# Performance work log

Measured on AMD Instinct MI355X. Metric: run time of the kernel, lower is better.

## Reference

```python
import jax, jax.numpy as jnp
import numpy as np

B, D, H, W = 32, 96, 96, 96
MAX_POINTS = 512
NUM_CLASSES = 512
# e3nn spherical-harmonic 'integral' normalization constants
C0 = 0.28209479177387814   # 1/(2*sqrt(pi))
C1 = 0.4886025119029199    # sqrt(3/(4*pi))
C2 = 0.6307831305050401    # sqrt(5/(4*pi))
SQ3 = 1.7320508075688772

# (multiplicity, irrep dim) blocks for each irreps layout
BLOCKS_IN = [(16, 1), (8, 3), (4, 5)]   # 16x0e + 8x1o + 4x2e = 60
BLOCKS_H1 = [(32, 1), (8, 3), (4, 5)]   # 76
BLOCKS_H2 = [(64, 1), (4, 3), (2, 5)]   # 86


def setup_inputs() -> dict:
    key = jax.random.key(0)
    ks = jax.random.split(key, 12)
    n = jax.random.normal
    return {
        "x": jax.random.uniform(ks[0], (B, 1, D, H, W), dtype=jnp.float32),
        "W1_0e": n(ks[1], (16, 32)), "W1_1o": n(ks[2], (8, 8)), "W1_2e": n(ks[3], (4, 4)),
        "W2_0e": n(ks[4], (32, 64)), "W2_1o": n(ks[5], (8, 4)), "W2_2e": n(ks[6], (4, 2)),
        "W3_0e": n(ks[7], (64, 128)),
        "fc1_w": n(ks[8], (128, 64)) * 0.05, "fc1_b": jnp.zeros((64,), jnp.float32),
        "fc2_w": n(ks[9], (64, NUM_CLASSES)) * 0.05, "fc2_b": jnp.zeros((NUM_CLASSES,), jnp.float32),
    }


def _topk_pointcloud(x):
    # topk sampling path: highest-density voxels (threshold filter is a no-op
    # for top-k when enough voxels pass, which holds here). x: (B,1,D,H,W)
    vol = x[:, 0]
    flat = vol.reshape(vol.shape[0], -1)
    vals, idx = jax.lax.top_k(flat, MAX_POINTS)          # (B,N)
    z = idx // (H * W)
    rem = idx % (H * W)
    y = rem // W
    xw = rem % W
    coords = jnp.stack([z, y, xw], axis=-1).astype(jnp.float32)  # (B,N,3)
    center = jnp.array([D, H, W], jnp.float32) / 2.0
    scale = float(max(D, H, W)) / 2.0
    points = (coords - center) / scale
    return points, vals


def _point_features(pts, vals):
    # pts: (B,N,3) normalized coords, vals: (B,N) densities -> (B,N,60)
    v = vals[..., None]
    denom = vals.sum(axis=1, keepdims=True)
    com = (pts * v).sum(axis=1) / jnp.maximum(denom, 1e-12)      # (B,3)
    c = pts - com[:, None, :]
    r = jnp.maximum(jnp.linalg.norm(c, axis=-1), 1e-6)           # r_safe (B,N)
    rr = r[..., None]
    d = c / rr                                                   # unit directions
    dx, dy, dz = d[..., 0], d[..., 1], d[..., 2]
    sh1 = C1 * d                                                 # l=1 SH, e3nn order (x,y,z)
    sh2 = C2 * jnp.stack([
        SQ3 * dx * dz,
        SQ3 * dx * dy,
        dy * dy - 0.5 * (dx * dx + dz * dz),
        SQ3 * dy * dz,
        0.5 * SQ3 * (dz * dz - dx * dx),
    ], axis=-1)                                                  # (B,N,5)
    l1pr = jnp.log1p(r)
    sh0 = jnp.full_like(vals, C0)
    scalars = jnp.stack([
        vals, r, sh0, vals * r, vals ** 2, l1pr, jnp.sqrt(vals + 1e-6),
        r ** 2, vals * sh0, jnp.exp(-r), vals ** 3, jnp.sqrt(r),
        vals * l1pr, jax.nn.sigmoid(vals), jax.nn.sigmoid(r), vals * r ** 2,
    ], axis=-1)                                                  # (B,N,16)
    vectors = jnp.concatenate([
        c, c * v, sh1, c * rr, d, d * v, c * v ** 2, sh1 * rr,
    ], axis=-1)                                                  # (B,N,24)
    tensors = jnp.concatenate([
        sh2, sh2 * v, sh2 * rr, sh2 * l1pr[..., None],
    ], axis=-1)                                                  # (B,N,20)
    return jnp.concatenate([scalars, vectors, tensors], axis=-1)


def _irreps_linear(feat, blocks, weights):
    # e3nn o3.Linear: block-diagonal per-irrep linear, one path per block,
    # path normalization 1/sqrt(mul_in). Blocks laid out mul-major.
    outs = []
    start = 0
    for (mul_in, dim), Wb in zip(blocks, weights):
        blk = feat[..., start:start + mul_in * dim]
        blk = blk.reshape(*feat.shape[:-1], mul_in, dim)
        out = jnp.einsum('bnui,uv->bnvi', blk, Wb) / np.sqrt(mul_in).astype(np.float32)
        outs.append(out.reshape(*feat.shape[:-1], -1))
        start += mul_in * dim
    return jnp.concatenate(outs, axis=-1)


def reference(x, W1_0e, W1_1o, W1_2e, W2_0e, W2_1o, W2_2e, W3_0e,
              fc1_w, fc1_b, fc2_w, fc2_b):
    pts, vals = _topk_pointcloud(x)
    feat = _point_features(pts, vals)                    # (B,512,60)
    h = _irreps_linear(feat, BLOCKS_IN, [W1_0e, W1_1o, W1_2e])   # (B,512,76)
    h = _irreps_linear(h, BLOCKS_H1, [W2_0e, W2_1o, W2_2e])      # (B,512,86)
    # layer3 -> 128x0e: only the 0e path exists, 1o/2e inputs are dropped
    h = _irreps_linear(h[..., :64], [(64, 1)], [W3_0e])          # (B,512,128)
    pooled = h.max(axis=1)                               # (B,128)
    hid = jax.nn.relu(pooled @ fc1_w + fc1_b)            # dropout is eval-mode identity
    logits = hid @ fc2_w + fc2_b
    return logits, feat
```

## Files before the change

kernel.cpp:

```cpp
#include <hip/hip_runtime.h>
#include <hip/hip_bf16.h>
#include <stdint.h>

#define NVOX   884736
#define NB     32
#define NPTS   512
#define CAP    4096
#define THRV   0.9990234375f
#define THR_TOP 0x3F7FFFFFu
#define BPB    216
#define SLOT   64
#define LBUF   80
#define NBUCK  128

#define C0c  0.28209479177387814f
#define C1c  0.4886025119029199f
#define C2c  0.6307831305050401f
#define SQ3c 1.7320508075688772f

typedef unsigned long long u64;
typedef unsigned int u32;

__global__ __launch_bounds__(256) void k_collect(const float* __restrict__ x,
                                                 u64* __restrict__ cand,
                                                 u32* __restrict__ counts) {
  const int b   = blockIdx.y;
  const int blk = blockIdx.x;
  const int tid = threadIdx.x;
  __shared__ u64 lbuf[LBUF];
  __shared__ int lcnt;
  if (tid == 0) lcnt = 0;
  __syncthreads();

  const float4* xb = reinterpret_cast<const float4*>(x + (size_t)b * NVOX);
  const int t0 = blk * 1024 + tid;
  float4 q[4];
  #pragma unroll
  for (int it = 0; it < 4; ++it) q[it] = xb[t0 + it * 256];

  #pragma unroll
  for (int it = 0; it < 4; ++it) {
    const float4 qq = q[it];
    const u32 base = (u32)(t0 + it * 256) * 4u;
    if (qq.x >= THRV) { int p = atomicAdd(&lcnt, 1); if (p < LBUF) lbuf[p] = ((u64)__float_as_uint(qq.x) << 32) | (u64)(~(base      )); }
    if (qq.y >= THRV) { int p = atomicAdd(&lcnt, 1); if (p < LBUF) lbuf[p] = ((u64)__float_as_uint(qq.y) << 32) | (u64)(~(base + 1u)); }
    if (qq.z >= THRV) { int p = atomicAdd(&lcnt, 1); if (p < LBUF) lbuf[p] = ((u64)__float_as_uint(qq.z) << 32) | (u64)(~(base + 2u)); }
    if (qq.w >= THRV) { int p = atomicAdd(&lcnt, 1); if (p < LBUF) lbuf[p] = ((u64)__float_as_uint(qq.w) << 32) | (u64)(~(base + 3u)); }
  }
  __syncthreads();

  const int slot = b * BPB + blk;
  const int n = lcnt;
  const int wn = (n <= SLOT) ? n : SLOT;
  if (tid < wn) cand[(size_t)slot * SLOT + tid] = lbuf[tid];
  if (tid == 0) counts[slot] = (n <= SLOT) ? (u32)n : (u32)(SLOT + 1);
}

__global__ __launch_bounds__(512) void k_select(const float* __restrict__ x,
                                                const u64* __restrict__ cand,
                                                const u32* __restrict__ counts,
                                                u64* __restrict__ sel,
                                                float* __restrict__ comvg) {
  const int b   = blockIdx.x;
  const int tid = threadIdx.x;

  __shared__ u64 lk[CAP];
  __shared__ u64 lk2[CAP];
  __shared__ u64 sk[NPTS];
  __shared__ u32 sA[256], sB[256];
  __shared__ u32 scnt[BPB], spref[BPB];
  __shared__ u32 bc[NBUCK], bbx[NBUCK], bp[NBUCK], bA[NBUCK], bB[NBUCK];
  __shared__ float rbuf[8][4];
  __shared__ int sbad, sC;
  __shared__ u32 sthr;

  u32 myc = 0;
  if (tid == 0) sbad = 0;
  if (tid < 256) { myc = (tid < BPB) ? counts[b * BPB + tid] : 0u; sA[tid] = myc; }
  __syncthreads();
  if (tid < BPB && myc > SLOT) atomicOr(&sbad, 1);
  u32 *ssrc = sA, *sdst = sB;
  for (int off = 1; off < 256; off <<= 1) {
    if (tid < 256) sdst[tid] = ssrc[tid] + ((tid >= off) ? ssrc[tid - off] : 0u);
    __syncthreads();
    u32* t = ssrc; ssrc = sdst; sdst = t;
  }
  const int total = (int)ssrc[255];
  if (tid < BPB) { scnt[tid] = myc; spref[tid] = ssrc[tid] - myc; }
  __syncthreads();

  int C;
  if (!sbad && total >= NPTS && total <= CAP) {
    C = total;
    for (int s = tid >> 1; s < BPB; s += 256) {
      const u32 c = scnt[s], p = spref[s];
      const u64* src = cand + (size_t)(b * BPB + s) * SLOT;
      for (u32 k = (u32)(tid & 1); k < c; k += 2) lk[p + k] = src[k];
    }
    __syncthreads();
  } else {
    u32* hist = reinterpret_cast<u32*>(lk);
    for (int i = tid; i < 4096; i += 512) hist[i] = 0u;
    __syncthreads();
    const u32* xb = reinterpret_cast<const u32*>(x) + (size_t)b * NVOX;
    for (int i = tid; i < NVOX; i += 512) {
      const u32 bits = xb[i];
      u32 key;
      if (bits >= 0x3F800000u) key = 0u;
      else { const u32 dd = THR_TOP - bits; key = dd >> 8; if (key > 4095u) key = 4095u; }
      atomicAdd(&hist[key], 1u);
    }
    __syncthreads();
    if (tid == 0) {
      u32 cum = 0; int kt = 4095;
      for (int k = 0; k < 4096; ++k) { cum += hist[k]; if (cum >= (u32)NPTS) { kt = k; break; } }
      sthr = (kt >= 4095) ? 0u : (0x3F800000u - ((u32)(kt + 1) << 8));
      sC = 0;
    }
    __syncthreads();
    const u32 thr = sthr;
    for (int i = tid; i < NVOX; i += 512) {
      const u32 bits = xb[i];
      if (bits >= thr) {
        const int p = atomicAdd(&sC, 1);
        if (p < CAP) lk[p] = ((u64)bits << 32) | (u64)(~(u32)i);
      }
    }
    __syncthreads();
    C = sC < CAP ? sC : CAP;
    __syncthreads();
  }

  if (tid < NBUCK) bc[tid] = 0u;
  __syncthreads();
  for (int i = tid; i < C; i += 512) {
    const u32 bits = (u32)(lk[i] >> 32);
    u32 bk = (THR_TOP - bits) >> 7; if (bk > (NBUCK - 1)) bk = NBUCK - 1;
    atomicAdd(&bc[bk], 1u);
  }
  __syncthreads();
  if (tid < NBUCK) bA[tid] = bc[tid];
  __syncthreads();
  u32 *bsrc = bA, *bdst = bB;
  for (int off = 1; off < NBUCK; off <<= 1) {
    if (tid < NBUCK) bdst[tid] = bsrc[tid] + ((tid >= off) ? bsrc[tid - off] : 0u);
    __syncthreads();
    u32* t = bsrc; bsrc = bdst; bdst = t;
  }
  if (tid < NBUCK) { bbx[tid] = bsrc[tid] - bc[tid]; bp[tid] = bsrc[tid] - bc[tid]; }
  __syncthreads();
  for (int i = tid; i < C; i += 512) {
    const u64 ki = lk[i];
    const u32 bits = (u32)(ki >> 32);
    u32 bk = (THR_TOP - bits) >> 7; if (bk > (NBUCK - 1)) bk = NBUCK - 1;
    const u32 p = atomicAdd(&bp[bk], 1u);
    lk2[p] = ki;
  }
  __syncthreads();
  for (int i = tid; i < C; i += 512) {
    const u64 ki = lk2[i];
    const u32 bits = (u32)(ki >> 32);
    u32 bk = (THR_TOP - bits) >> 7; if (bk > (NBUCK - 1)) bk = NBUCK - 1;
    const u32 lo = bbx[bk], hi = lo + bc[bk];
    int rank = (int)lo;
    for (u32 j = lo; j < hi; ++j) rank += (lk2[j] > ki) ? 1 : 0;
    if (rank < NPTS) sk[rank] = ki;
  }
  __syncthreads();

  const u64 key = sk[tid];
  sel[(size_t)b * NPTS + tid] = key;

  const u32 bits = (u32)(key >> 32);
  const u32 idx  = ~((u32)key);
  const float v  = __uint_as_float(bits);
  const u32 z = idx / 9216u, rem = idx % 9216u, yy = rem / 96u, xw = rem % 96u;
  const float p0 = ((float)z  - 48.f) / 48.f;
  const float p1 = ((float)yy - 48.f) / 48.f;
  const float p2 = ((float)xw - 48.f) / 48.f;
  float sv = v, s0 = p0 * v, s1 = p1 * v, s2 = p2 * v;
  for (int off = 32; off > 0; off >>= 1) {
    sv += __shfl_down(sv, off);
    s0 += __shfl_down(s0, off);
    s1 += __shfl_down(s1, off);
    s2 += __shfl_down(s2, off);
  }
  const int w = tid >> 6, ln = tid & 63;
  if (ln == 0) { rbuf[w][0] = sv; rbuf[w][1] = s0; rbuf[w][2] = s1; rbuf[w][3] = s2; }
  __syncthreads();
  if (tid == 0) {
    float tv = 0.f, t0s = 0.f, t1s = 0.f, t2s = 0.f;
    for (int wv = 0; wv < 8; ++wv) { tv += rbuf[wv][0]; t0s += rbuf[wv][1]; t1s += rbuf[wv][2]; t2s += rbuf[wv][3]; }
    const float dnm = fmaxf(tv, 1e-12f);
    comvg[b * 4 + 0] = t0s / dnm; comvg[b * 4 + 1] = t1s / dnm;
    comvg[b * 4 + 2] = t2s / dnm; comvg[b * 4 + 3] = 0.f;
  }
}

__global__ __launch_bounds__(512) void k_featpool(const u64* __restrict__ sel,
                                                  const float* __restrict__ comvg,
                                                  const float* __restrict__ W1,
                                                  const float* __restrict__ W2,
                                                  const float* __restrict__ W3,
                                                  float* __restrict__ ppart,
                                                  float* __restrict__ dout) {
  const int p8  = blockIdx.x;
  const int b   = blockIdx.y;
  const int tid = threadIdx.x;
  __shared__ float Tm[16 * 64];
  __shared__ float Ms[16 * 128];
  __shared__ __align__(16) float fs[64][20];
  __shared__ float pr[4][128];

  const float s1c = 1.0f / (4.0f * sqrtf(32.0f));
  for (int e = tid; e < 16 * 64; e += 512) {
    const int u = e >> 6, j = e & 63;
    float s = 0.f;
    for (int k = 0; k < 32; ++k) s += W1[u * 32 + k] * W2[k * 64 + j];
    Tm[e] = s * s1c;
  }
  __syncthreads();
  for (int e = tid; e < 16 * 128; e += 512) {
    const int u = e >> 7, vv = e & 127;
    float s = 0.f;
    for (int j = 0; j < 64; ++j) s += Tm[u * 64 + j] * W3[j * 128 + vv];
    Ms[e] = s * 0.125f;
  }

  const int pl = tid >> 3, cg = tid & 7;
  const int gp = b * NPTS + p8 * 64 + pl;
  const u64 key = sel[gp];
  const u32 bits = (u32)(key >> 32);
  const u32 idx  = ~((u32)key);
  const float v  = __uint_as_float(bits);
  const u32 z = idx / 9216u, rem = idx % 9216u, yy = rem / 96u, xw = rem % 96u;
  const float4 cm = reinterpret_cast<const float4*>(comvg)[b];
  const float c0 = ((float)z  - 48.f) / 48.f - cm.x;
  const float c1 = ((float)yy - 48.f) / 48.f - cm.y;
  const float c2 = ((float)xw - 48.f) / 48.f - cm.z;
  const float r = fmaxf(sqrtf(c0 * c0 + c1 * c1 + c2 * c2), 1e-6f);
  const float inv = 1.0f / r;
  const float d0 = c0 * inv, d1 = c1 * inv, d2 = c2 * inv;
  const float v2 = v * v;
  const float rr2 = r * r;
  const float l1 = log1pf(r);
  const float er = expf(-r);
  const float sgv = 1.0f / (1.0f + expf(-v));
  const float sgr = 1.0f / (1.0f + expf(-r));

  float f[60];
  f[0]=v;      f[1]=r;      f[2]=C0c;     f[3]=v*r;
  f[4]=v2;     f[5]=l1;     f[6]=sqrtf(v + 1e-6f); f[7]=rr2;
  f[8]=v*C0c;  f[9]=er;     f[10]=v2*v;   f[11]=sqrtf(r);
  f[12]=v*l1;  f[13]=sgv;   f[14]=sgr;    f[15]=v*rr2;
  f[16]=c0;        f[17]=c1;        f[18]=c2;
  f[19]=c0*v;      f[20]=c1*v;      f[21]=c2*v;
  f[22]=C1c*d0;    f[23]=C1c*d1;    f[24]=C1c*d2;
  f[25]=c0*r;      f[26]=c1*r;      f[27]=c2*r;
  f[28]=d0;        f[29]=d1;        f[30]=d2;
  f[31]=d0*v;      f[32]=d1*v;      f[33]=d2*v;
  f[34]=c0*v2;     f[35]=c1*v2;     f[36]=c2*v2;
  f[37]=C1c*d0*r;  f[38]=C1c*d1*r;  f[39]=C1c*d2*r;
  const float t0 = C2c * (SQ3c * d0 * d2);
  const float t1 = C2c * (SQ3c * d0 * d1);
  const float t2_ = C2c * (d1 * d1 - 0.5f * (d0 * d0 + d2 * d2));
  const float t3 = C2c * (SQ3c * d1 * d2);
  const float t4 = C2c * (0.5f * SQ3c * (d2 * d2 - d0 * d0));
  f[40]=t0;     f[41]=t1;     f[42]=t2_;     f[43]=t3;     f[44]=t4;
  f[45]=t0*v;   f[46]=t1*v;   f[47]=t2_*v;   f[48]=t3*v;   f[49]=t4*v;
  f[50]=t0*r;   f[51]=t1*r;   f[52]=t2_*r;   f[53]=t3*r;   f[54]=t4*r;
  f[55]=t0*l1;  f[56]=t1*l1;  f[57]=t2_*l1;  f[58]=t3*l1;  f[59]=t4*l1;

  float4* ob = reinterpret_cast<float4*>(dout + 16384 + (size_t)gp * 60);
  #pragma unroll
  for (int k = 0; k < 15; ++k)
    if ((k & 7) == cg) ob[k] = make_float4(f[4*k], f[4*k+1], f[4*k+2], f[4*k+3]);

  #pragma unroll
  for (int k = 0; k < 4; ++k)
    if (k == cg) *reinterpret_cast<float4*>(&fs[pl][k * 4]) =
        make_float4(f[4*k], f[4*k+1], f[4*k+2], f[4*k+3]);
  __syncthreads();

  const int g = tid >> 7, vv = tid & 127;
  float mreg[16];
  #pragma unroll
  for (int u = 0; u < 16; ++u) mreg[u] = Ms[u * 128 + vv];
  float pm = -3.4e38f;
  for (int n = g; n < 64; n += 4) {
    const float4 a0 = *reinterpret_cast<const float4*>(&fs[n][0]);
    const float4 a1 = *reinterpret_cast<const float4*>(&fs[n][4]);
    const float4 a2 = *reinterpret_cast<const float4*>(&fs[n][8]);
    const float4 a3 = *reinterpret_cast<const float4*>(&fs[n][12]);
    float acc = a0.x*mreg[0] + a0.y*mreg[1] + a0.z*mreg[2] + a0.w*mreg[3]
              + a1.x*mreg[4] + a1.y*mreg[5] + a1.z*mreg[6] + a1.w*mreg[7]
              + a2.x*mreg[8] + a2.y*mreg[9] + a2.z*mreg[10]+ a2.w*mreg[11]
              + a3.x*mreg[12]+ a3.y*mreg[13]+ a3.z*mreg[14]+ a3.w*mreg[15];
    pm = fmaxf(pm, acc);
  }
  pr[g][vv] = pm;
  __syncthreads();
  if (g == 0)
    ppart[((size_t)b * 8 + p8) * 128 + vv] =
        fmaxf(fmaxf(pr[0][vv], pr[1][vv]), fmaxf(pr[2][vv], pr[3][vv]));
}

__global__ __launch_bounds__(512) void k_head(const float* __restrict__ ppart,
                                              const float* __restrict__ fc1w,
                                              const float* __restrict__ fc1b,
                                              const float* __restrict__ fc2w,
                                              const float* __restrict__ fc2b,
                                              float* __restrict__ dout) {
  const int b = blockIdx.x;
  const int t = threadIdx.x;
  __shared__ float pl[128];
  __shared__ float hid[64];
  if (t < 128) {
    float m = -3.4e38f;
    #pragma unroll
    for (int k = 0; k < 8; ++k) m = fmaxf(m, ppart[((size_t)b * 8 + k) * 128 + t]);
    pl[t] = m;
  }
  __syncthreads();
  if (t < 64) {
    float sh = fc1b[t];
    for (int u = 0; u < 128; ++u) sh += pl[u] * fc1w[u * 64 + t];
    hid[t] = fmaxf(sh, 0.f);
  }
  __syncthreads();
  float sl = fc2b[t];
  for (int j = 0; j < 64; ++j) sl += hid[j] * fc2w[j * 512 + t];
  dout[b * 512 + t] = sl;
}

extern "C" void kernel_launch(void* const* d_in, const int* in_sizes, int n_in,
                              void* d_out, int out_size, void* d_ws, size_t ws_size,
                              hipStream_t stream) {
  const float* x    = (const float*)d_in[0];
  const float* W1   = (const float*)d_in[1];
  const float* W2   = (const float*)d_in[4];
  const float* W3   = (const float*)d_in[7];
  const float* fc1w = (const float*)d_in[8];
  const float* fc1b = (const float*)d_in[9];
  const float* fc2w = (const float*)d_in[10];
  const float* fc2b = (const float*)d_in[11];
  float* out = (float*)d_out;

  uint8_t* ws = (uint8_t*)d_ws;
  u32*   counts = (u32*)ws;
  u64*   cand   = (u64*)(ws + 0x10000);
  u64*   sel    = (u64*)(ws + 0x400000);
  float* comv   = (float*)(ws + 0x420000);
  float* ppart  = (float*)(ws + 0x421000);

  dim3 g1(BPB, NB);
  k_collect<<<g1, 256, 0, stream>>>(x, cand, counts);
  k_select<<<NB, 512, 0, stream>>>(x, cand, counts, sel, comv);
  dim3 g3(8, NB);
  k_featpool<<<g3, 512, 0, stream>>>(sel, comv, W1, W2, W3, ppart, out);
  k_head<<<NB, 512, 0, stream>>>(ppart, fc1w, fc1b, fc2w, fc2b, out);
}
```

Baseline: 45.21 us.

## Fuse select, feature, pooling and head kernels into one per-batch worker kernel

```diff
diff --git a/kernel.cpp b/kernel.cpp
--- a/kernel.cpp
+++ b/kernel.cpp
@@ -56,26 +56,55 @@
   if (tid == 0) counts[slot] = (n <= SLOT) ? (u32)n : (u32)(SLOT + 1);
 }
 
-__global__ __launch_bounds__(512) void k_select(const float* __restrict__ x,
+__global__ __launch_bounds__(512) void k_worker(const float* __restrict__ x,
                                                 const u64* __restrict__ cand,
                                                 const u32* __restrict__ counts,
-                                                u64* __restrict__ sel,
-                                                float* __restrict__ comvg) {
+                                                const float* __restrict__ W1,
+                                                const float* __restrict__ W2,
+                                                const float* __restrict__ W3,
+                                                const float* __restrict__ fc1w,
+                                                const float* __restrict__ fc1b,
+                                                const float* __restrict__ fc2w,
+                                                const float* __restrict__ fc2b,
+                                                float* __restrict__ dout) {
   const int b   = blockIdx.x;
   const int tid = threadIdx.x;
 
-  __shared__ u64 lk[CAP];
-  __shared__ u64 lk2[CAP];
+  __shared__ __align__(16) char arena[65536];
   __shared__ u64 sk[NPTS];
+  __shared__ float Tm[16 * 64];
+  __shared__ float Ms[16 * 128];
+  __shared__ float pr[4][128];
+  __shared__ float pl[128];
+  __shared__ float hid[64];
   __shared__ u32 sA[256], sB[256];
   __shared__ u32 scnt[BPB], spref[BPB];
   __shared__ u32 bc[NBUCK], bbx[NBUCK], bp[NBUCK], bA[NBUCK], bB[NBUCK];
   __shared__ float rbuf[8][4];
+  __shared__ float comv[4];
   __shared__ int sbad, sC;
   __shared__ u32 sthr;
 
+  u64* lk  = reinterpret_cast<u64*>(arena);
+  u64* lk2 = reinterpret_cast<u64*>(arena + 32768);
+
+  const float s1c = 1.0f / (4.0f * sqrtf(32.0f));
+  for (int e = tid; e < 16 * 64; e += 512) {
+    const int u = e >> 6, j = e & 63;
+    float s = 0.f;
+    for (int k = 0; k < 32; ++k) s += W1[u * 32 + k] * W2[k * 64 + j];
+    Tm[e] = s * s1c;
+  }
+  if (tid == 0) sbad = 0;
+  __syncthreads();
+  for (int e = tid; e < 16 * 128; e += 512) {
+    const int u = e >> 7, vv = e & 127;
+    float s = 0.f;
+    for (int j = 0; j < 64; ++j) s += Tm[u * 64 + j] * W3[j * 128 + vv];
+    Ms[e] = s * 0.125f;
+  }
+
   u32 myc = 0;
-  if (tid == 0) sbad = 0;
   if (tid < 256) { myc = (tid < BPB) ? counts[b * BPB + tid] : 0u; sA[tid] = myc; }
   __syncthreads();
   if (tid < BPB && myc > SLOT) atomicOr(&sbad, 1);
@@ -169,8 +198,6 @@
   __syncthreads();
 
   const u64 key = sk[tid];
-  sel[(size_t)b * NPTS + tid] = key;
-
   const u32 bits = (u32)(key >> 32);
   const u32 idx  = ~((u32)key);
   const float v  = __uint_as_float(bits);
@@ -178,66 +205,32 @@
   const float p0 = ((float)z  - 48.f) / 48.f;
   const float p1 = ((float)yy - 48.f) / 48.f;
   const float p2 = ((float)xw - 48.f) / 48.f;
-  float sv = v, s0 = p0 * v, s1 = p1 * v, s2 = p2 * v;
-  for (int off = 32; off > 0; off >>= 1) {
-    sv += __shfl_down(sv, off);
-    s0 += __shfl_down(s0, off);
-    s1 += __shfl_down(s1, off);
-    s2 += __shfl_down(s2, off);
-  }
-  const int w = tid >> 6, ln = tid & 63;
-  if (ln == 0) { rbuf[w][0] = sv; rbuf[w][1] = s0; rbuf[w][2] = s1; rbuf[w][3] = s2; }
-  __syncthreads();
-  if (tid == 0) {
-    float tv = 0.f, t0s = 0.f, t1s = 0.f, t2s = 0.f;
-    for (int wv = 0; wv < 8; ++wv) { tv += rbuf[wv][0]; t0s += rbuf[wv][1]; t1s += rbuf[wv][2]; t2s += rbuf[wv][3]; }
-    const float dnm = fmaxf(tv, 1e-12f);
-    comvg[b * 4 + 0] = t0s / dnm; comvg[b * 4 + 1] = t1s / dnm;
-    comvg[b * 4 + 2] = t2s / dnm; comvg[b * 4 + 3] = 0.f;
-  }
-}
-
-__global__ __launch_bounds__(512) void k_featpool(const u64* __restrict__ sel,
-                                                  const float* __restrict__ comvg,
-                                                  const float* __restrict__ W1,
-                                                  const float* __restrict__ W2,
-                                                  const float* __restrict__ W3,
-                                                  float* __restrict__ ppart,
-                                                  float* __restrict__ dout) {
-  const int p8  = blockIdx.x;
-  const int b   = blockIdx.y;
-  const int tid = threadIdx.x;
-  __shared__ float Tm[16 * 64];
-  __shared__ float Ms[16 * 128];
-  __shared__ __align__(16) float fs[64][20];
-  __shared__ float pr[4][128];
-
-  const float s1c = 1.0f / (4.0f * sqrtf(32.0f));
-  for (int e = tid; e < 16 * 64; e += 512) {
-    const int u = e >> 6, j = e & 63;
-    float s = 0.f;
-    for (int k = 0; k < 32; ++k) s += W1[u * 32 + k] * W2[k * 64 + j];
-    Tm[e] = s * s1c;
-  }
-  __syncthreads();
-  for (int e = tid; e < 16 * 128; e += 512) {
-    const int u = e >> 7, vv = e & 127;
-    float s = 0.f;
-    for (int j = 0; j < 64; ++j) s += Tm[u * 64 + j] * W3[j * 128 + vv];
-    Ms[e] = s * 0.125f;
-  }
-
-  const int pl = tid >> 3, cg = tid & 7;
-  const int gp = b * NPTS + p8 * 64 + pl;
-  const u64 key = sel[gp];
-  const u32 bits = (u32)(key >> 32);
-  const u32 idx  = ~((u32)key);
-  const float v  = __uint_as_float(bits);
-  const u32 z = idx / 9216u, rem = idx % 9216u, yy = rem / 96u, xw = rem % 96u;
-  const float4 cm = reinterpret_cast<const float4*>(comvg)[b];
-  const float c0 = ((float)z  - 48.f) / 48.f - cm.x;
-  const float c1 = ((float)yy - 48.f) / 48.f - cm.y;
-  const float c2 = ((float)xw - 48.f) / 48.f - cm.z;
+
+  {
+    float sv = v, s0 = p0 * v, s1 = p1 * v, s2 = p2 * v;
+    for (int off = 32; off > 0; off >>= 1) {
+      sv += __shfl_down(sv, off);
+      s0 += __shfl_down(s0, off);
+      s1 += __shfl_down(s1, off);
+      s2 += __shfl_down(s2, off);
+    }
+    const int w = tid >> 6, ln = tid & 63;
+    if (ln == 0) { rbuf[w][0] = sv; rbuf[w][1] = s0; rbuf[w][2] = s1; rbuf[w][3] = s2; }
+    __syncthreads();
+    if (tid == 0) {
+      float tv = 0.f, t0s = 0.f, t1s = 0.f, t2s = 0.f;
+      for (int wv = 0; wv < 8; ++wv) { tv += rbuf[wv][0]; t0s += rbuf[wv][1]; t1s += rbuf[wv][2]; t2s += rbuf[wv][3]; }
+      const float dnm = fmaxf(tv, 1e-12f);
+      comv[0] = t0s / dnm; comv[1] = t1s / dnm; comv[2] = t2s / dnm;
+    }
+    __syncthreads();
+  }
+
+  float (*fs)[20] = reinterpret_cast<float(*)[20]>(arena);
+
+  const float c0 = p0 - comv[0];
+  const float c1 = p1 - comv[1];
+  const float c2 = p2 - comv[2];
   const float r = fmaxf(sqrtf(c0 * c0 + c1 * c1 + c2 * c2), 1e-6f);
   const float inv = 1.0f / r;
   const float d0 = c0 * inv, d1 = c1 * inv, d2 = c2 * inv;
@@ -271,15 +264,13 @@
   f[50]=t0*r;   f[51]=t1*r;   f[52]=t2_*r;   f[53]=t3*r;   f[54]=t4*r;
   f[55]=t0*l1;  f[56]=t1*l1;  f[57]=t2_*l1;  f[58]=t3*l1;  f[59]=t4*l1;
 
-  float4* ob = reinterpret_cast<float4*>(dout + 16384 + (size_t)gp * 60);
-  #pragma unroll
-  for (int k = 0; k < 15; ++k)
-    if ((k & 7) == cg) ob[k] = make_float4(f[4*k], f[4*k+1], f[4*k+2], f[4*k+3]);
+  float4* ob = reinterpret_cast<float4*>(dout + 16384 + ((size_t)b * NPTS + tid) * 60);
+  #pragma unroll
+  for (int k = 0; k < 15; ++k) ob[k] = make_float4(f[4*k], f[4*k+1], f[4*k+2], f[4*k+3]);
 
   #pragma unroll
   for (int k = 0; k < 4; ++k)
-    if (k == cg) *reinterpret_cast<float4*>(&fs[pl][k * 4]) =
-        make_float4(f[4*k], f[4*k+1], f[4*k+2], f[4*k+3]);
+    *reinterpret_cast<float4*>(&fs[tid][k * 4]) = make_float4(f[4*k], f[4*k+1], f[4*k+2], f[4*k+3]);
   __syncthreads();
 
   const int g = tid >> 7, vv = tid & 127;
@@ -287,7 +278,7 @@
   #pragma unroll
   for (int u = 0; u < 16; ++u) mreg[u] = Ms[u * 128 + vv];
   float pm = -3.4e38f;
-  for (int n = g; n < 64; n += 4) {
+  for (int n = g; n < NPTS; n += 4) {
     const float4 a0 = *reinterpret_cast<const float4*>(&fs[n][0]);
     const float4 a1 = *reinterpret_cast<const float4*>(&fs[n][4]);
     const float4 a2 = *reinterpret_cast<const float4*>(&fs[n][8]);
@@ -300,37 +291,18 @@
   }
   pr[g][vv] = pm;
   __syncthreads();
-  if (g == 0)
-    ppart[((size_t)b * 8 + p8) * 128 + vv] =
-        fmaxf(fmaxf(pr[0][vv], pr[1][vv]), fmaxf(pr[2][vv], pr[3][vv]));
-}
-
-__global__ __launch_bounds__(512) void k_head(const float* __restrict__ ppart,
-                                              const float* __restrict__ fc1w,
-                                              const float* __restrict__ fc1b,
-                                              const float* __restrict__ fc2w,
-                                              const float* __restrict__ fc2b,
-                                              float* __restrict__ dout) {
-  const int b = blockIdx.x;
-  const int t = threadIdx.x;
-  __shared__ float pl[128];
-  __shared__ float hid[64];
-  if (t < 128) {
-    float m = -3.4e38f;
-    #pragma unroll
-    for (int k = 0; k < 8; ++k) m = fmaxf(m, ppart[((size_t)b * 8 + k) * 128 + t]);
-    pl[t] = m;
-  }
-  __syncthreads();
-  if (t < 64) {
-    float sh = fc1b[t];
-    for (int u = 0; u < 128; ++u) sh += pl[u] * fc1w[u * 64 + t];
-    hid[t] = fmaxf(sh, 0.f);
-  }
-  __syncthreads();
-  float sl = fc2b[t];
-  for (int j = 0; j < 64; ++j) sl += hid[j] * fc2w[j * 512 + t];
-  dout[b * 512 + t] = sl;
+  if (g == 0) pl[vv] = fmaxf(fmaxf(pr[0][vv], pr[1][vv]), fmaxf(pr[2][vv], pr[3][vv]));
+  __syncthreads();
+
+  if (tid < 64) {
+    float sh = fc1b[tid];
+    for (int u = 0; u < 128; ++u) sh += pl[u] * fc1w[u * 64 + tid];
+    hid[tid] = fmaxf(sh, 0.f);
+  }
+  __syncthreads();
+  float sl = fc2b[tid];
+  for (int j = 0; j < 64; ++j) sl += hid[j] * fc2w[j * 512 + tid];
+  dout[b * 512 + tid] = sl;
 }
 
 extern "C" void kernel_launch(void* const* d_in, const int* in_sizes, int n_in,
@@ -347,16 +319,11 @@
   float* out = (float*)d_out;
 
   uint8_t* ws = (uint8_t*)d_ws;
-  u32*   counts = (u32*)ws;
-  u64*   cand   = (u64*)(ws + 0x10000);
-  u64*   sel    = (u64*)(ws + 0x400000);
-  float* comv   = (float*)(ws + 0x420000);
-  float* ppart  = (float*)(ws + 0x421000);
+  u32* counts = (u32*)ws;
+  u64* cand   = (u64*)(ws + 0x10000);
 
   dim3 g1(BPB, NB);
   k_collect<<<g1, 256, 0, stream>>>(x, cand, counts);
-  k_select<<<NB, 512, 0, stream>>>(x, cand, counts, sel, comv);
-  dim3 g3(8, NB);
-  k_featpool<<<g3, 512, 0, stream>>>(sel, comv, W1, W2, W3, ppart, out);
-  k_head<<<NB, 512, 0, stream>>>(ppart, fc1w, fc1b, fc2w, fc2b, out);
+  k_worker<<<NB, 512, 0, stream>>>(x, cand, counts, W1, W2, W3,
+                                   fc1w, fc1b, fc2w, fc2b, out);
 }
```

After: 58.01 us. 28.3% more time.
